# Kernel optimization log

Hardware: AMD Instinct MI355X
Metric: run time of the kernel (lower is better)

Reference implementation:

```python
import jax, jax.numpy as jnp
import numpy as np

E = 65536      # num edges
T = 262144     # num triplets
H = 128        # hidden_channels
D = 64         # int_emb_size
C = 8          # basis_emb_size
NR = 6         # num_radial
NS = 7         # num_spherical
NB = 6         # len(bt_list) = num_BT + 1
BT_LIST = (-1, 0, 1, 2, 3, 4)
NBS = 1        # num_before_skip (also used for after-skip list in original code)


def setup_inputs() -> dict:
    key = jax.random.key(0)
    ks = iter(jax.random.split(key, 40))
    s = 0.05
    p = lambda shape: jax.random.normal(next(ks), shape, dtype=jnp.float32) * s
    inp = dict(
        x=jax.random.normal(next(ks), (E, H), dtype=jnp.float32),
        rbf=jax.random.normal(next(ks), (E, NR), dtype=jnp.float32),
        sbf=jax.random.normal(next(ks), (T, NS * NR), dtype=jnp.float32),
        idx_kj=jax.random.randint(next(ks), (T,), 0, E),
        idx_ji=jax.random.randint(next(ks), (T,), 0, E),
        bt=jax.random.randint(next(ks), (E,), 0, 5),
        lambda_d=1,
        alpha=jnp.float32(0.7),
        # per-branch stacked weights (6 branches)
        W_kj=p((NB, H, H)), b_kj=jnp.zeros((NB, H), jnp.float32),
        W_rbf1=p((NB, NR, C)), W_rbf2=p((NB, C, H)),
        W_sbf1=p((NB, NS * NR, C)), W_sbf2=p((NB, C, D)),
        W_down=p((NB, H, D)),
        W_ji=p((H, H)), b_ji=jnp.zeros((H,), jnp.float32),
        W_up=p((D, H)),
        rb1_w=p((NBS, H, H)), rb1_b=jnp.zeros((NBS, H), jnp.float32),
        rb2_w=p((NBS, H, H)), rb2_b=jnp.zeros((NBS, H), jnp.float32),
        W_lin=p((H, H)), b_lin=jnp.zeros((H,), jnp.float32),
        ra1_w=p((NBS, H, H)), ra1_b=jnp.zeros((NBS, H), jnp.float32),
        ra2_w=p((NBS, H, H)), ra2_b=jnp.zeros((NBS, H), jnp.float32),
    )
    return inp


def reference(x, rbf, sbf, idx_kj, idx_ji, bt, lambda_d, alpha,
              W_kj, b_kj, W_rbf1, W_rbf2, W_sbf1, W_sbf2, W_down,
              W_ji, b_ji, W_up, rb1_w, rb1_b, rb2_w, rb2_b,
              W_lin, b_lin, ra1_w, ra1_b, ra2_w, ra2_b):
    act = jax.nn.silu

    x_ji = act(x @ W_ji + b_ji)                                  # [E,H]

    # per-branch edge transforms, vectorized over the 6 branches (axis b)
    tmp = act(jnp.einsum('eh,bhg->beg', x, W_kj) + b_kj[:, None, :])   # [B,E,H]
    rbf_p = jnp.einsum('er,brc->bec', rbf, W_rbf1)                     # [B,E,C]
    rbf_p = jnp.einsum('bec,bcg->beg', rbf_p, W_rbf2)                  # [B,E,H]
    tmp = tmp * rbf_p
    down = act(jnp.einsum('beh,bhd->bed', tmp, W_down))                # [B,E,D]

    sbf_p = jnp.einsum('ts,bsc->btc', sbf, W_sbf1)                     # [B,T,C]
    sbf_p = jnp.einsum('btc,bcd->btd', sbf_p, W_sbf2)                  # [B,T,D]

    spe = down[:, idx_kj, :] * sbf_p                                   # [B,T,D]

    # last branch scattered with weight alpha
    x_kj_tot = alpha * jax.ops.segment_sum(spe[-1], idx_ji, num_segments=E)

    # per band-type masked scatter with weight (1 - alpha)
    bt_trip = bt[idx_kj]                                               # [T]
    for b, btv in enumerate(BT_LIST):
        m = (bt_trip == btv).astype(x.dtype)[:, None]
        x_kj_tot = x_kj_tot + (1.0 - alpha) * jax.ops.segment_sum(
            spe[b] * m, idx_ji, num_segments=E)

    x_kj = act(x_kj_tot @ W_up)                                        # [E,H]
    h = x_ji + x_kj
    for i in range(rb1_w.shape[0]):
        h = h + act(act(h @ rb1_w[i] + rb1_b[i]) @ rb2_w[i] + rb2_b[i])
    h = act(h @ W_lin + b_lin) + x
    for i in range(ra1_w.shape[0]):
        h = h + act(act(h @ ra1_w[i] + ra1_b[i]) @ ra2_w[i] + ra2_b[i])
    return h
```

## Files before the change

### kernel.cpp

```cpp
#include <hip/hip_runtime.h>
#include <hip/hip_bf16.h>
#include <stdint.h>

typedef __bf16 bf16_t;
typedef bf16_t bf16x8 __attribute__((ext_vector_type(8)));
typedef bf16_t bf16x2 __attribute__((ext_vector_type(2)));
typedef float f32x4 __attribute__((ext_vector_type(4)));

#define E_N 65536
#define T_N 262144
#define CAP 16
#define OVF_MAX T_N

#define ESET_BYTES 61440
#define PSET_BYTES 36864

__device__ __forceinline__ float silu_f(float v) {
  return v / (1.0f + __expf(-v));
}

__device__ __forceinline__ int permrow(int n) {
  return (n & ~31) | ((n & 1) << 4) | ((n & 30) >> 1);
}

__device__ __forceinline__ uint32_t pack_bf16(float a, float b) {
  union { bf16x2 h; uint32_t u; } u;
  u.h[0] = (bf16_t)a; u.h[1] = (bf16_t)b;
  return u.u;
}

__device__ __forceinline__ void g2l16(const void* g, void* l) {
  __builtin_amdgcn_global_load_lds(
      (const __attribute__((address_space(1))) void*)g,
      (__attribute__((address_space(3))) void*)l, 16, 0, 0);
}

template<int CHUNKS>
__device__ __forceinline__ void dma_copy(const char* g, char* l, int wv, int lane) {
#pragma unroll
  for (int c = 0; c < CHUNKS / 4; ++c) {
    const int off = (c * 4 + wv) * 1024 + lane * 16;
    g2l16(g + off, l + off);
  }
}

#define VMCNT0()  asm volatile("s_waitcnt vmcnt(0)" ::: "memory")

template<int KI, int NTJ>
__device__ __forceinline__ void gemm_tile(const bf16_t* A, const bf16_t* B,
                                          int mb, int nb, int l16, int q,
                                          f32x4 (&acc)[2][NTJ]) {
#pragma unroll
  for (int kt = 0; kt < KI; ++kt) {
    const int sw = ((kt * 4 + q) ^ l16) << 3;
    bf16x8 a0 = *(const bf16x8*)(A + ((mb + l16) << 7) + sw);
    bf16x8 a1 = *(const bf16x8*)(A + ((mb + 16 + l16) << 7) + sw);
#pragma unroll
    for (int tj = 0; tj < NTJ; ++tj) {
      bf16x8 b = *(const bf16x8*)(B + ((nb + tj * 16 + l16) << 7) + sw);
      acc[0][tj] = __builtin_amdgcn_mfma_f32_16x16x32_bf16(a0, b, acc[0][tj], 0, 0, 0);
      acc[1][tj] = __builtin_amdgcn_mfma_f32_16x16x32_bf16(a1, b, acc[1][tj], 0, 0, 0);
    }
  }
}

template<int C4>
__device__ __forceinline__ void stage_x(bf16_t* dst, const float* src, int tid) {
  const float4* g = (const float4*)src;
#pragma unroll
  for (int i = tid; i < 64 * C4; i += 256) {
    const int row = i / C4, c4 = i % C4;
    float4 v = g[i];
    bf16_t t[4] = {(bf16_t)v.x, (bf16_t)v.y, (bf16_t)v.z, (bf16_t)v.w};
    *(uint2*)(dst + (row << 7) + ((((c4 >> 1) ^ (row & 15)) << 3) | ((c4 & 1) << 2))) =
        *(const uint2*)t;
  }
}

__global__ void prep_kernel(
    const float* __restrict__ W_ji, const float* __restrict__ W_kj,
    const float* __restrict__ W_down, const float* __restrict__ W_up,
    const float* __restrict__ rb1, const float* __restrict__ rb2,
    const float* __restrict__ W_lin, const float* __restrict__ ra1,
    const float* __restrict__ ra2, const float* __restrict__ W_rbf1,
    const float* __restrict__ W_rbf2,
    const float* __restrict__ b_ji, const float* __restrict__ b_kj,
    const float* __restrict__ rb1_b, const float* __restrict__ rb2_b,
    const float* __restrict__ b_lin, const float* __restrict__ ra1_b,
    const float* __restrict__ ra2_b,
    char* __restrict__ esets, char* __restrict__ psets)
{
  const int tid = threadIdx.x;
  const int blk = blockIdx.x;

  if (blk < 88) {
    const int item = blk * 256 + tid;
    const int m = item >> 11, w = item & 2047;
    const int n = w >> 4, k8 = w & 15;
    const float* src; char* img;
    if (m == 0)      { src = W_ji;             img = esets; }
    else if (m <= 5) { src = W_kj + m * 16384; img = esets + m * ESET_BYTES; }
    else if (m == 6) { src = rb1;   img = psets + 1 * PSET_BYTES; }
    else if (m == 7) { src = rb2;   img = psets + 2 * PSET_BYTES; }
    else if (m == 8) { src = W_lin; img = psets + 3 * PSET_BYTES; }
    else if (m == 9) { src = ra1;   img = psets + 4 * PSET_BYTES; }
    else             { src = ra2;   img = psets + 5 * PSET_BYTES; }
    bf16_t t[8];
#pragma unroll
    for (int j = 0; j < 8; ++j) t[j] = (bf16_t)src[(k8 * 8 + j) * 128 + n];
    const int row = permrow(n);
    *(uint4*)((bf16_t*)img + (row << 7) + ((k8 ^ (row & 15)) << 3)) = *(const uint4*)t;
  } else if (blk < 108) {
    const int item = (blk - 88) * 256 + tid;
    const int m = item >> 10, w = item & 1023;
    const int n = w >> 4, k8 = w & 15;
    const float* src = W_down + (m + 1) * 8192;
    bf16_t* img = (bf16_t*)(esets + (m + 1) * ESET_BYTES + 32768);
    bf16_t t[8];
#pragma unroll
    for (int j = 0; j < 8; ++j) t[j] = (bf16_t)src[(k8 * 8 + j) * 64 + n];
    const int row = permrow(n);
    *(uint4*)(img + (row << 7) + ((k8 ^ (row & 15)) << 3)) = *(const uint4*)t;
  } else if (blk < 112) {
    const int item = (blk - 108) * 256 + tid;
    const int n = item >> 3, k8 = item & 7;
    bf16_t t[8];
#pragma unroll
    for (int j = 0; j < 8; ++j) t[j] = (bf16_t)W_up[(k8 * 8 + j) * 128 + n];
    const int row = permrow(n);
    *(uint4*)((bf16_t*)psets + (row << 7) + ((k8 ^ (row & 15)) << 3)) = *(const uint4*)t;
  } else if (blk < 115) {
    const int o = (blk - 112) * 256 + tid;
    if (o < 640) {
      const int b = o >> 7, n = o & 127;
      bf16_t t[8];
#pragma unroll
      for (int r = 0; r < 6; ++r) {
        const float* w1 = W_rbf1 + (b + 1) * 48 + r * 8;
        const float* w2 = W_rbf2 + (b + 1) * 1024 + n;
        float s = 0.f;
#pragma unroll
        for (int c = 0; c < 8; ++c) s += w1[c] * w2[c * 128];
        t[r] = (bf16_t)s;
      }
      t[6] = (bf16_t)0.f; t[7] = (bf16_t)0.f;
      bf16_t* img = (bf16_t*)(esets + (b + 1) * ESET_BYTES + 49152);
      const int row = permrow(n);
      const uint4 z = {0, 0, 0, 0};
      *(uint4*)(img + row * 40)      = *(const uint4*)t;
      *(uint4*)(img + row * 40 + 8)  = z;
      *(uint4*)(img + row * 40 + 16) = z;
      *(uint4*)(img + row * 40 + 24) = z;
    }
  } else {
    const int n = tid & 127;
    for (int v = (tid >> 7); v < 11; v += 2) {
      float val; char* dst;
      if (v == 0)      { val = b_ji[n];          dst = esets + 59392; }
      else if (v <= 5) { val = b_kj[v * 128 + n]; dst = esets + v * ESET_BYTES + 59392; }
      else {
        const float* bs = (v == 6) ? rb1_b : (v == 7) ? rb2_b :
                          (v == 8) ? b_lin : (v == 9) ? ra1_b : ra2_b;
        val = bs[n]; dst = psets + (v - 5) * PSET_BYTES + 32768;
      }
      ((float*)dst)[n] = val;
    }
  }
}

__global__ __launch_bounds__(256, 1)
void edge_kernel(const float* __restrict__ x, const float* __restrict__ rbf,
                 const char* __restrict__ esets,
                 bf16_t* __restrict__ x_ji_out, bf16_t* __restrict__ down)
{
  __shared__ __align__(16) bf16_t xA[64 * 128];
  __shared__ __align__(16) bf16_t tmpA[64 * 128];
  __shared__ __align__(16) bf16_t rbfA[64 * 40];
  __shared__ __align__(16) char Wset[2][ESET_BYTES];

  const int tid = threadIdx.x;
  const int lane = tid & 63, wv = tid >> 6;
  const int q = lane >> 4, l16 = lane & 15;
  const int mb = (wv >> 1) * 32, nb = (wv & 1) * 64;
  const int R = blockIdx.x * 64;

  stage_x<32>(xA, x + (size_t)R * 128, tid);
  if (tid < 64) {
    const float* rg = rbf + (size_t)(R + tid) * 6;
    bf16_t t[8] = {(bf16_t)rg[0], (bf16_t)rg[1], (bf16_t)rg[2],
                   (bf16_t)rg[3], (bf16_t)rg[4], (bf16_t)rg[5],
                   (bf16_t)0.f, (bf16_t)0.f};
    const uint4 z = {0, 0, 0, 0};
    *(uint4*)(rbfA + tid * 40)      = *(const uint4*)t;
    *(uint4*)(rbfA + tid * 40 + 8)  = z;
    *(uint4*)(rbfA + tid * 40 + 16) = z;
    *(uint4*)(rbfA + tid * 40 + 24) = z;
  }
  VMCNT0();
  dma_copy<60>(esets,              (char*)Wset[0], wv, lane);
  dma_copy<60>(esets + ESET_BYTES, (char*)Wset[1], wv, lane);
  asm volatile("s_waitcnt vmcnt(15)" ::: "memory");
  __syncthreads();

  for (int br = 0; br < 6; ++br) {
    const char* slot = Wset[br & 1];
    const bf16_t* Wm  = (const bf16_t*)slot;
    const bf16_t* Wdn = (const bf16_t*)(slot + 32768);
    const bf16_t* Wcb = (const bf16_t*)(slot + 49152);
    const float* biasS = (const float*)(slot + 59392);

    f32x4 acc[2][4] = {};
    gemm_tile<4, 4>(xA, Wm, mb, nb, l16, q, acc);

    if (br == 0) {
#pragma unroll
      for (int ti = 0; ti < 2; ++ti)
#pragma unroll
        for (int r = 0; r < 4; ++r) {
          const int row = mb + ti * 16 + q * 4 + r;
#pragma unroll
          for (int gl = 0; gl < 2; ++gl) {
            const int col0 = nb + gl * 32 + 2 * l16;
            const float2 b2 = *(const float2*)&biasS[col0];
            *(uint32_t*)&x_ji_out[(size_t)(R + row) * 128 + col0] =
                pack_bf16(silu_f(acc[ti][2 * gl][r] + b2.x),
                          silu_f(acc[ti][2 * gl + 1][r] + b2.y));
          }
        }
    } else {
      f32x4 accr[2][4] = {};
      {
        bf16x8 a0 = *(const bf16x8*)(rbfA + (mb + l16) * 40 + q * 8);
        bf16x8 a1 = *(const bf16x8*)(rbfA + (mb + 16 + l16) * 40 + q * 8);
#pragma unroll
        for (int tj = 0; tj < 4; ++tj) {
          bf16x8 b = *(const bf16x8*)(Wcb + (nb + tj * 16 + l16) * 40 + q * 8);
          accr[0][tj] = __builtin_amdgcn_mfma_f32_16x16x32_bf16(a0, b, accr[0][tj], 0, 0, 0);
          accr[1][tj] = __builtin_amdgcn_mfma_f32_16x16x32_bf16(a1, b, accr[1][tj], 0, 0, 0);
        }
      }
#pragma unroll
      for (int ti = 0; ti < 2; ++ti)
#pragma unroll
        for (int r = 0; r < 4; ++r) {
          const int row = mb + ti * 16 + q * 4 + r;
#pragma unroll
          for (int gl = 0; gl < 2; ++gl) {
            const int col0 = nb + gl * 32 + 2 * l16;
            const float2 b2 = *(const float2*)&biasS[col0];
            const float v0 = silu_f(acc[ti][2 * gl][r] + b2.x) * accr[ti][2 * gl][r];
            const float v1 = silu_f(acc[ti][2 * gl + 1][r] + b2.y) * accr[ti][2 * gl + 1][r];
            *(uint32_t*)&tmpA[(row << 7) + ((((col0 >> 3) ^ (row & 15)) << 3) | (col0 & 7))] =
                pack_bf16(v0, v1);
          }
        }
      __syncthreads();

      const int nb2 = (wv & 1) * 32;
      f32x4 acc2[2][2] = {};
      gemm_tile<4, 2>(tmpA, Wdn, mb, nb2, l16, q, acc2);
#pragma unroll
      for (int ti = 0; ti < 2; ++ti)
#pragma unroll
        for (int r = 0; r < 4; ++r) {
          const int row = mb + ti * 16 + q * 4 + r;
          const int col0 = nb2 + 2 * l16;
          *(uint32_t*)&down[((size_t)(br - 1) * E_N + R + row) * 64 + col0] =
              pack_bf16(silu_f(acc2[ti][0][r]), silu_f(acc2[ti][1][r]));
        }
    }

    VMCNT0();
    __syncthreads();
    if (br < 4)
      dma_copy<60>(esets + (size_t)(br + 2) * ESET_BYTES, (char*)Wset[br & 1], wv, lane);
  }
}

__global__ __launch_bounds__(256, 4)
void c8_kernel(const float* __restrict__ sbf, const int* __restrict__ idx_kj,
               const int* __restrict__ idx_ji, const int* __restrict__ bt,
               const float* __restrict__ Wsbf1,
               float* __restrict__ c8g, uint32_t* __restrict__ meta,
               int* __restrict__ cnt, int* __restrict__ list,
               int* __restrict__ ovf)
{
  __shared__ float s_sbf[64 * 44];
  __shared__ float s_W1[2016];
  __shared__ float s_c8[64 * 16];
  __shared__ int s_bs[64];

  const int tid = threadIdx.x;
  const int base = blockIdx.x * 64;

  for (int i = tid; i < 2016; i += 256) s_W1[i] = Wsbf1[i];
  if (tid < 64) {
    const int t = base + tid;
    const int kj = idx_kj[t];
    const int ji = idx_ji[t];
    const int bs = bt[kj] + 1;
    s_bs[tid] = bs;
    meta[t] = (uint32_t)kj | ((uint32_t)bs << 16);
    const int pos = atomicAdd(&cnt[ji], 1);
    if (pos < CAP) {
      list[ji * CAP + pos] = t;
    } else {
      const int o = atomicAdd(&ovf[0], 1);
      if (o < OVF_MAX) { ovf[2 + 2 * o] = t; ovf[2 + 2 * o + 1] = ji; }
    }
  }
  {
    const float2* sg = (const float2*)(sbf + (size_t)base * 42);
    for (int i = tid; i < 64 * 21; i += 256) {
      const int r = i / 21, c2 = i - r * 21;
      const float2 v = sg[i];
      s_sbf[r * 44 + c2 * 2] = v.x;
      s_sbf[r * 44 + c2 * 2 + 1] = v.y;
    }
  }
  __syncthreads();

  {
    const int i = tid >> 2;
    const int brr = (tid >> 1) & 1;
    const int cg = tid & 1;
    const int b = brr ? s_bs[i] : 5;
    const float* w = &s_W1[b * 336 + cg * 4];
    const float* sb = &s_sbf[i * 44];
    float a0 = 0.f, a1 = 0.f, a2 = 0.f, a3 = 0.f;
#pragma unroll
    for (int s = 0; s < 42; ++s) {
      const float sv = sb[s];
      const float* ws = w + s * 8;
      a0 += sv * ws[0]; a1 += sv * ws[1]; a2 += sv * ws[2]; a3 += sv * ws[3];
    }
    float* dc = &s_c8[i * 16 + brr * 8 + cg * 4];
    dc[0] = a0; dc[1] = a1; dc[2] = a2; dc[3] = a3;
  }
  __syncthreads();

  {
    const float4* s4 = (const float4*)s_c8;
    float4* g4 = (float4*)(c8g + (size_t)base * 16);
    g4[tid] = s4[tid];
  }
}

__global__ __launch_bounds__(256, 8)
void gather_kernel(const int* __restrict__ cnt, const int* __restrict__ list,
                   const uint32_t* __restrict__ meta, const float* __restrict__ c8g,
                   const float* __restrict__ Wsbf2, const bf16_t* __restrict__ down,
                   const float* __restrict__ alpha_p, const int* __restrict__ ovf,
                   float* __restrict__ xkj)
{
  __shared__ float sW2[3072];
  for (int i = threadIdx.x; i < 3072; i += 256) sW2[i] = Wsbf2[i];
  __syncthreads();

  const int e = blockIdx.x * 4 + (threadIdx.x >> 6);
  const int j = threadIdx.x & 63;
  const float alpha = alpha_p[0], oma = 1.f - alpha;
  const float* w5 = &sW2[5 * 512 + j];

  float acc = 0.f;
  int n = cnt[e];
  if (n > CAP) n = CAP;
#pragma unroll 2
  for (int k = 0; k < n; ++k) {
    const int t = __builtin_amdgcn_readfirstlane(list[e * CAP + k]);
    const uint32_t m = __builtin_amdgcn_readfirstlane(meta[t]);
    const int kj = m & 0xffff;
    const int b  = m >> 16;
    const float g5 = (float)down[((size_t)4 * E_N + kj) * 64 + j];
    const float gb = (float)down[((size_t)(b - 1) * E_N + kj) * 64 + j];
    const float* cp = c8g + (size_t)t * 16;
    float d5 = 0.f, db = 0.f;
#pragma unroll
    for (int c = 0; c < 8; ++c) {
      d5 += cp[c]     * w5[c * 64];
      db += cp[8 + c] * sW2[b * 512 + c * 64 + j];
    }
    acc += alpha * g5 * d5 + oma * gb * db;
  }

  const int oc = ovf[0];
  for (int k = 0; k < oc; ++k) {
    const int ji = ovf[2 + 2 * k + 1];
    if (ji != e) continue;
    const int t = ovf[2 + 2 * k];
    const uint32_t m = meta[t];
    const int kj = m & 0xffff;
    const int b  = m >> 16;
    const float g5 = (float)down[((size_t)4 * E_N + kj) * 64 + j];
    const float gb = (float)down[((size_t)(b - 1) * E_N + kj) * 64 + j];
    const float* cp = c8g + (size_t)t * 16;
    float d5 = 0.f, db = 0.f;
#pragma unroll
    for (int c = 0; c < 8; ++c) {
      d5 += cp[c]     * w5[c * 64];
      db += cp[8 + c] * sW2[b * 512 + c * 64 + j];
    }
    acc += alpha * g5 * d5 + oma * gb * db;
  }

  xkj[(size_t)e * 64 + j] = acc;
}

__global__ __launch_bounds__(256, 1)
void epi_kernel(const float* __restrict__ x, const bf16_t* __restrict__ x_ji,
                const float* __restrict__ xkj, const char* __restrict__ psets,
                float* __restrict__ out)
{
  __shared__ __align__(16) bf16_t bufA[64 * 128];
  __shared__ __align__(16) bf16_t bufB[64 * 128];
  __shared__ __align__(16) char Wset[2][PSET_BYTES];

  const int tid = threadIdx.x;
  const int lane = tid & 63, wv = tid >> 6;
  const int q = lane >> 4, l16 = lane & 15;
  const int mb = (wv >> 1) * 32, nb = (wv & 1) * 64;
  const int R = blockIdx.x * 64;

  stage_x<16>(bufA, xkj + (size_t)R * 64, tid);
  VMCNT0();
  dma_copy<36>(psets,              (char*)Wset[0], wv, lane);
  dma_copy<36>(psets + PSET_BYTES, (char*)Wset[1], wv, lane);
  asm volatile("s_waitcnt vmcnt(9)" ::: "memory");
  __syncthreads();

  f32x4 hreg[2][4];
  {
    f32x4 acc[2][4] = {};
    gemm_tile<2, 4>(bufA, (const bf16_t*)Wset[0], mb, nb, l16, q, acc);
#pragma unroll
    for (int ti = 0; ti < 2; ++ti)
#pragma unroll
      for (int r = 0; r < 4; ++r) {
        const int row = mb + ti * 16 + q * 4 + r;
#pragma unroll
        for (int gl = 0; gl < 2; ++gl) {
          const int col0 = nb + gl * 32 + 2 * l16;
          union { uint32_t u; bf16x2 h; } xj;
          xj.u = *(const uint32_t*)&x_ji[(size_t)(R + row) * 128 + col0];
          const float h0 = (float)xj.h[0] + silu_f(acc[ti][2 * gl][r]);
          const float h1 = (float)xj.h[1] + silu_f(acc[ti][2 * gl + 1][r]);
          hreg[ti][2 * gl][r] = h0;
          hreg[ti][2 * gl + 1][r] = h1;
          *(uint32_t*)&bufB[(row << 7) + ((((col0 >> 3) ^ (row & 15)) << 3) | (col0 & 7))] =
              pack_bf16(h0, h1);
        }
      }
  }
  VMCNT0();
  __syncthreads();
  dma_copy<36>(psets + 2 * PSET_BYTES, (char*)Wset[0], wv, lane);

#define EPI_STAGE(K, ASRC, BODY)                                                 \
  {                                                                              \
    const char* slot_ = Wset[(K) & 1];                                           \
    const float* biasS = (const float*)(slot_ + 32768);                          \
    f32x4 acc[2][4] = {};                                                        \
    gemm_tile<4, 4>(ASRC, (const bf16_t*)slot_, mb, nb, l16, q, acc);            \
    _Pragma("unroll")                                                            \
    for (int ti = 0; ti < 2; ++ti)                                               \
      _Pragma("unroll")                                                          \
      for (int r = 0; r < 4; ++r) {                                              \
        const int row = mb + ti * 16 + q * 4 + r;                                \
        _Pragma("unroll")                                                        \
        for (int gl = 0; gl < 2; ++gl) {                                         \
          const int col0 = nb + gl * 32 + 2 * l16;                               \
          const float2 b2 = *(const float2*)&biasS[col0];                        \
          const float g0 = acc[ti][2 * gl][r] + b2.x;                            \
          const float g1 = acc[ti][2 * gl + 1][r] + b2.y;                        \
          BODY                                                                   \
        }                                                                        \
      }                                                                          \
  }                                                                              \
  VMCNT0();                                                                      \
  __syncthreads();                                                               \
  if ((K) + 2 <= 5)                                                              \
    dma_copy<36>(psets + ((K) + 2) * PSET_BYTES, (char*)Wset[(K) & 1], wv, lane);

  EPI_STAGE(1, bufB, {
    *(uint32_t*)&bufA[(row << 7) + ((((col0 >> 3) ^ (row & 15)) << 3) | (col0 & 7))] =
        pack_bf16(silu_f(g0), silu_f(g1));
  })

  EPI_STAGE(2, bufA, {
    const float h0 = hreg[ti][2 * gl][r] + silu_f(g0);
    const float h1 = hreg[ti][2 * gl + 1][r] + silu_f(g1);
    hreg[ti][2 * gl][r] = h0; hreg[ti][2 * gl + 1][r] = h1;
    *(uint32_t*)&bufB[(row << 7) + ((((col0 >> 3) ^ (row & 15)) << 3) | (col0 & 7))] =
        pack_bf16(h0, h1);
  })

  EPI_STAGE(3, bufB, {
    const float2 xv = *(const float2*)&x[(size_t)(R + row) * 128 + col0];
    const float h0 = silu_f(g0) + xv.x;
    const float h1 = silu_f(g1) + xv.y;
    hreg[ti][2 * gl][r] = h0; hreg[ti][2 * gl + 1][r] = h1;
    *(uint32_t*)&bufA[(row << 7) + ((((col0 >> 3) ^ (row & 15)) << 3) | (col0 & 7))] =
        pack_bf16(h0, h1);
  })

  EPI_STAGE(4, bufA, {
    *(uint32_t*)&bufB[(row << 7) + ((((col0 >> 3) ^ (row & 15)) << 3) | (col0 & 7))] =
        pack_bf16(silu_f(g0), silu_f(g1));
  })

  EPI_STAGE(5, bufB, {
    float2 o;
    o.x = hreg[ti][2 * gl][r] + silu_f(g0);
    o.y = hreg[ti][2 * gl + 1][r] + silu_f(g1);
    *(float2*)&out[(size_t)(R + row) * 128 + col0] = o;
  })
#undef EPI_STAGE
}

extern "C" void kernel_launch(void* const* d_in, const int* in_sizes, int n_in,
                              void* d_out, int out_size, void* d_ws, size_t ws_size,
                              hipStream_t stream)
{
  (void)in_sizes; (void)n_in; (void)out_size; (void)ws_size;
  const float* x      = (const float*)d_in[0];
  const float* rbf    = (const float*)d_in[1];
  const float* sbf    = (const float*)d_in[2];
  const int*   idx_kj = (const int*)d_in[3];
  const int*   idx_ji = (const int*)d_in[4];
  const int*   bt     = (const int*)d_in[5];
  const float* alpha  = (const float*)d_in[7];
  const float* W_kj   = (const float*)d_in[8];
  const float* b_kj   = (const float*)d_in[9];
  const float* W_rbf1 = (const float*)d_in[10];
  const float* W_rbf2 = (const float*)d_in[11];
  const float* W_sbf1 = (const float*)d_in[12];
  const float* W_sbf2 = (const float*)d_in[13];
  const float* W_down = (const float*)d_in[14];
  const float* W_ji   = (const float*)d_in[15];
  const float* b_ji   = (const float*)d_in[16];
  const float* W_up   = (const float*)d_in[17];
  const float* rb1_w  = (const float*)d_in[18];
  const float* rb1_b  = (const float*)d_in[19];
  const float* rb2_w  = (const float*)d_in[20];
  const float* rb2_b  = (const float*)d_in[21];
  const float* W_lin  = (const float*)d_in[22];
  const float* b_lin  = (const float*)d_in[23];
  const float* ra1_w  = (const float*)d_in[24];
  const float* ra1_b  = (const float*)d_in[25];
  const float* ra2_w  = (const float*)d_in[26];
  const float* ra2_b  = (const float*)d_in[27];

  char* ws = (char*)d_ws;
  bf16_t* down   = (bf16_t*)(ws);
  bf16_t* x_ji   = (bf16_t*)(ws + 41943040);
  float*  xkj    = (float*) (ws + 58720256);
  char*   esets  = ws + 75497472;
  char*   psets  = ws + 75866112;
  float*    c8g  = (float*)   (ws + 76087296);
  uint32_t* meta = (uint32_t*)(ws + 92864512);
  int*      list = (int*)     (ws + 93913088);
  int*      cnt  = (int*)     (ws + 98107392);
  int*      ovf  = (int*)     (ws + 98369536);

  hipMemsetAsync(cnt, 0, 262144 + 8, stream);
  prep_kernel<<<116, 256, 0, stream>>>(W_ji, W_kj, W_down, W_up, rb1_w, rb2_w,
                                       W_lin, ra1_w, ra2_w, W_rbf1, W_rbf2,
                                       b_ji, b_kj, rb1_b, rb2_b, b_lin,
                                       ra1_b, ra2_b, esets, psets);
  edge_kernel<<<E_N / 64, 256, 0, stream>>>(x, rbf, esets, x_ji, down);
  c8_kernel<<<T_N / 64, 256, 0, stream>>>(sbf, idx_kj, idx_ji, bt, W_sbf1,
                                          c8g, meta, cnt, list, ovf);
  gather_kernel<<<E_N / 4 / 64, 256, 0, stream>>>(cnt, list, meta, c8g, W_sbf2,
                                                  down, alpha, ovf, xkj);
  epi_kernel<<<E_N / 64, 256, 0, stream>>>(x, x_ji, xkj, psets, (float*)d_out);
}
```

Measured before the change: 362.9 us.

## Enlarge edge and epilogue tiles to 128 rows with 512 threads and split weight images

Result: slower. 417.9 us (+15.2%).

```diff
diff --git a/kernel.cpp b/kernel.cpp
--- a/kernel.cpp
+++ b/kernel.cpp
@@ -12,9 +12,6 @@
 #define CAP 16
 #define OVF_MAX T_N
 
-#define ESET_BYTES 61440
-#define PSET_BYTES 36864
-
 __device__ __forceinline__ float silu_f(float v) {
   return v / (1.0f + __expf(-v));
 }
@@ -36,15 +33,22 @@
 }
 
 template<int CHUNKS>
-__device__ __forceinline__ void dma_copy(const char* g, char* l, int wv, int lane) {
-#pragma unroll
-  for (int c = 0; c < CHUNKS / 4; ++c) {
-    const int off = (c * 4 + wv) * 1024 + lane * 16;
+__device__ __forceinline__ void dma8(const char* g, char* l, int wv, int lane) {
+#pragma unroll
+  for (int c = 0; c < CHUNKS / 8; ++c) {
+    const int off = (c * 8 + wv) * 1024 + lane * 16;
     g2l16(g + off, l + off);
   }
 }
 
-#define VMCNT0()  asm volatile("s_waitcnt vmcnt(0)" ::: "memory")
+#define VMCNT0()   asm volatile("s_waitcnt vmcnt(0)" ::: "memory")
+#define S_VMCNT_(n) asm volatile("s_waitcnt vmcnt(" #n ")" ::: "memory")
+#define S_VMCNT(n) S_VMCNT_(n)
+#define BARRIER() do {                                          \
+    asm volatile("s_waitcnt lgkmcnt(0)" ::: "memory");          \
+    __builtin_amdgcn_s_barrier();                               \
+    __builtin_amdgcn_sched_barrier(0);                          \
+  } while (0)
 
 template<int KI, int NTJ>
 __device__ __forceinline__ void gemm_tile(const bf16_t* A, const bf16_t* B,
@@ -64,11 +68,11 @@
   }
 }
 
-template<int C4>
+template<int C4, int NT>
 __device__ __forceinline__ void stage_x(bf16_t* dst, const float* src, int tid) {
   const float4* g = (const float4*)src;
 #pragma unroll
-  for (int i = tid; i < 64 * C4; i += 256) {
+  for (int i = tid; i < 128 * C4; i += NT) {
     const int row = i / C4, c4 = i % C4;
     float4 v = g[i];
     bf16_t t[4] = {(bf16_t)v.x, (bf16_t)v.y, (bf16_t)v.z, (bf16_t)v.w};
@@ -84,11 +88,8 @@
     const float* __restrict__ W_lin, const float* __restrict__ ra1,
     const float* __restrict__ ra2, const float* __restrict__ W_rbf1,
     const float* __restrict__ W_rbf2,
-    const float* __restrict__ b_ji, const float* __restrict__ b_kj,
-    const float* __restrict__ rb1_b, const float* __restrict__ rb2_b,
-    const float* __restrict__ b_lin, const float* __restrict__ ra1_b,
-    const float* __restrict__ ra2_b,
-    char* __restrict__ esets, char* __restrict__ psets)
+    char* __restrict__ wm_img, char* __restrict__ wdn_img,
+    char* __restrict__ pset, bf16_t* __restrict__ wcb)
 {
   const int tid = threadIdx.x;
   const int blk = blockIdx.x;
@@ -98,13 +99,13 @@
     const int m = item >> 11, w = item & 2047;
     const int n = w >> 4, k8 = w & 15;
     const float* src; char* img;
-    if (m == 0)      { src = W_ji;             img = esets; }
-    else if (m <= 5) { src = W_kj + m * 16384; img = esets + m * ESET_BYTES; }
-    else if (m == 6) { src = rb1;   img = psets + 1 * PSET_BYTES; }
-    else if (m == 7) { src = rb2;   img = psets + 2 * PSET_BYTES; }
-    else if (m == 8) { src = W_lin; img = psets + 3 * PSET_BYTES; }
-    else if (m == 9) { src = ra1;   img = psets + 4 * PSET_BYTES; }
-    else             { src = ra2;   img = psets + 5 * PSET_BYTES; }
+    if (m == 0)      { src = W_ji;             img = wm_img; }
+    else if (m <= 5) { src = W_kj + m * 16384; img = wm_img + m * 32768; }
+    else if (m == 6) { src = rb1;   img = pset + 1 * 32768; }
+    else if (m == 7) { src = rb2;   img = pset + 2 * 32768; }
+    else if (m == 8) { src = W_lin; img = pset + 3 * 32768; }
+    else if (m == 9) { src = ra1;   img = pset + 4 * 32768; }
+    else             { src = ra2;   img = pset + 5 * 32768; }
     bf16_t t[8];
 #pragma unroll
     for (int j = 0; j < 8; ++j) t[j] = (bf16_t)src[(k8 * 8 + j) * 128 + n];
@@ -115,7 +116,7 @@
     const int m = item >> 10, w = item & 1023;
     const int n = w >> 4, k8 = w & 15;
     const float* src = W_down + (m + 1) * 8192;
-    bf16_t* img = (bf16_t*)(esets + (m + 1) * ESET_BYTES + 32768);
+    bf16_t* img = (bf16_t*)(wdn_img + m * 16384);
     bf16_t t[8];
 #pragma unroll
     for (int j = 0; j < 8; ++j) t[j] = (bf16_t)src[(k8 * 8 + j) * 64 + n];
@@ -128,8 +129,8 @@
 #pragma unroll
     for (int j = 0; j < 8; ++j) t[j] = (bf16_t)W_up[(k8 * 8 + j) * 128 + n];
     const int row = permrow(n);
-    *(uint4*)((bf16_t*)psets + (row << 7) + ((k8 ^ (row & 15)) << 3)) = *(const uint4*)t;
-  } else if (blk < 115) {
+    *(uint4*)((bf16_t*)pset + (row << 7) + ((k8 ^ (row & 15)) << 3)) = *(const uint4*)t;
+  } else {
     const int o = (blk - 112) * 256 + tid;
     if (o < 640) {
       const int b = o >> 7, n = o & 127;
@@ -144,137 +145,144 @@
         t[r] = (bf16_t)s;
       }
       t[6] = (bf16_t)0.f; t[7] = (bf16_t)0.f;
-      bf16_t* img = (bf16_t*)(esets + (b + 1) * ESET_BYTES + 49152);
-      const int row = permrow(n);
-      const uint4 z = {0, 0, 0, 0};
-      *(uint4*)(img + row * 40)      = *(const uint4*)t;
-      *(uint4*)(img + row * 40 + 8)  = z;
-      *(uint4*)(img + row * 40 + 16) = z;
-      *(uint4*)(img + row * 40 + 24) = z;
-    }
-  } else {
-    const int n = tid & 127;
-    for (int v = (tid >> 7); v < 11; v += 2) {
-      float val; char* dst;
-      if (v == 0)      { val = b_ji[n];          dst = esets + 59392; }
-      else if (v <= 5) { val = b_kj[v * 128 + n]; dst = esets + v * ESET_BYTES + 59392; }
-      else {
-        const float* bs = (v == 6) ? rb1_b : (v == 7) ? rb2_b :
-                          (v == 8) ? b_lin : (v == 9) ? ra1_b : ra2_b;
-        val = bs[n]; dst = psets + (v - 5) * PSET_BYTES + 32768;
-      }
-      ((float*)dst)[n] = val;
-    }
-  }
-}
-
-__global__ __launch_bounds__(256, 1)
+      *(uint4*)(wcb + (b * 128 + n) * 8) = *(const uint4*)t;
+    }
+  }
+}
+
+__global__ __launch_bounds__(512, 2)
 void edge_kernel(const float* __restrict__ x, const float* __restrict__ rbf,
-                 const char* __restrict__ esets,
+                 const char* __restrict__ wm_img, const char* __restrict__ wdn_img,
+                 const bf16_t* __restrict__ wcb,
+                 const float* __restrict__ b_ji, const float* __restrict__ b_kj,
                  bf16_t* __restrict__ x_ji_out, bf16_t* __restrict__ down)
 {
-  __shared__ __align__(16) bf16_t xA[64 * 128];
-  __shared__ __align__(16) bf16_t tmpA[64 * 128];
-  __shared__ __align__(16) bf16_t rbfA[64 * 40];
-  __shared__ __align__(16) char Wset[2][ESET_BYTES];
+  __shared__ __align__(16) bf16_t xA[128 * 128];
+  __shared__ __align__(16) bf16_t tmpA[128 * 128];
+  __shared__ __align__(16) bf16_t Wm[2][128 * 128];
+  __shared__ __align__(16) bf16_t Wdn[64 * 128];
+  __shared__ __align__(16) bf16_t rbfS[128 * 8];
+  __shared__ __align__(16) bf16_t wcbS[5 * 128 * 8];
+  __shared__ __align__(16) float biasLDS[6 * 128];
 
   const int tid = threadIdx.x;
   const int lane = tid & 63, wv = tid >> 6;
   const int q = lane >> 4, l16 = lane & 15;
-  const int mb = (wv >> 1) * 32, nb = (wv & 1) * 64;
-  const int R = blockIdx.x * 64;
-
-  stage_x<32>(xA, x + (size_t)R * 128, tid);
-  if (tid < 64) {
+  const int mb = (wv >> 1) * 32, nb = (wv & 1) * 64, nb2 = (wv & 1) * 32;
+  const int R = blockIdx.x * 128;
+
+  stage_x<32, 512>(xA, x + (size_t)R * 128, tid);
+  if (tid < 128) {
     const float* rg = rbf + (size_t)(R + tid) * 6;
-    bf16_t t[8] = {(bf16_t)rg[0], (bf16_t)rg[1], (bf16_t)rg[2],
-                   (bf16_t)rg[3], (bf16_t)rg[4], (bf16_t)rg[5],
-                   (bf16_t)0.f, (bf16_t)0.f};
-    const uint4 z = {0, 0, 0, 0};
-    *(uint4*)(rbfA + tid * 40)      = *(const uint4*)t;
-    *(uint4*)(rbfA + tid * 40 + 8)  = z;
-    *(uint4*)(rbfA + tid * 40 + 16) = z;
-    *(uint4*)(rbfA + tid * 40 + 24) = z;
-  }
+    const float2 r01 = *(const float2*)(rg);
+    const float2 r23 = *(const float2*)(rg + 2);
+    const float2 r45 = *(const float2*)(rg + 4);
+    bf16_t t[8] = {(bf16_t)r01.x, (bf16_t)r01.y, (bf16_t)r23.x, (bf16_t)r23.y,
+                   (bf16_t)r45.x, (bf16_t)r45.y, (bf16_t)0.f, (bf16_t)0.f};
+    *(uint4*)(rbfS + tid * 8) = *(const uint4*)t;
+  }
+  for (int i = tid; i < 640; i += 512)
+    ((uint4*)wcbS)[i] = ((const uint4*)wcb)[i];
+  for (int i = tid; i < 768; i += 512) {
+    const int b = i >> 7, n = i & 127;
+    biasLDS[i] = (b == 0) ? b_ji[n] : b_kj[b * 128 + n];
+  }
+
   VMCNT0();
-  dma_copy<60>(esets,              (char*)Wset[0], wv, lane);
-  dma_copy<60>(esets + ESET_BYTES, (char*)Wset[1], wv, lane);
-  asm volatile("s_waitcnt vmcnt(15)" ::: "memory");
-  __syncthreads();
-
-  for (int br = 0; br < 6; ++br) {
-    const char* slot = Wset[br & 1];
-    const bf16_t* Wm  = (const bf16_t*)slot;
-    const bf16_t* Wdn = (const bf16_t*)(slot + 32768);
-    const bf16_t* Wcb = (const bf16_t*)(slot + 49152);
-    const float* biasS = (const float*)(slot + 59392);
-
+  dma8<32>(wm_img,          (char*)Wm[0], wv, lane);
+  dma8<32>(wm_img + 32768,  (char*)Wm[1], wv, lane);
+  dma8<16>(wdn_img,         (char*)Wdn,   wv, lane);
+  S_VMCNT(6);
+  BARRIER();
+
+  {
     f32x4 acc[2][4] = {};
-    gemm_tile<4, 4>(xA, Wm, mb, nb, l16, q, acc);
-
-    if (br == 0) {
-#pragma unroll
-      for (int ti = 0; ti < 2; ++ti)
-#pragma unroll
-        for (int r = 0; r < 4; ++r) {
-          const int row = mb + ti * 16 + q * 4 + r;
-#pragma unroll
-          for (int gl = 0; gl < 2; ++gl) {
-            const int col0 = nb + gl * 32 + 2 * l16;
-            const float2 b2 = *(const float2*)&biasS[col0];
-            *(uint32_t*)&x_ji_out[(size_t)(R + row) * 128 + col0] =
-                pack_bf16(silu_f(acc[ti][2 * gl][r] + b2.x),
-                          silu_f(acc[ti][2 * gl + 1][r] + b2.y));
-          }
-        }
-    } else {
-      f32x4 accr[2][4] = {};
-      {
-        bf16x8 a0 = *(const bf16x8*)(rbfA + (mb + l16) * 40 + q * 8);
-        bf16x8 a1 = *(const bf16x8*)(rbfA + (mb + 16 + l16) * 40 + q * 8);
-#pragma unroll
-        for (int tj = 0; tj < 4; ++tj) {
-          bf16x8 b = *(const bf16x8*)(Wcb + (nb + tj * 16 + l16) * 40 + q * 8);
-          accr[0][tj] = __builtin_amdgcn_mfma_f32_16x16x32_bf16(a0, b, accr[0][tj], 0, 0, 0);
-          accr[1][tj] = __builtin_amdgcn_mfma_f32_16x16x32_bf16(a1, b, accr[1][tj], 0, 0, 0);
+    gemm_tile<4, 4>(xA, Wm[0], mb, nb, l16, q, acc);
+    const float* bi = biasLDS;
+#pragma unroll
+    for (int ti = 0; ti < 2; ++ti)
+#pragma unroll
+      for (int r = 0; r < 4; ++r) {
+        const int row = mb + ti * 16 + q * 4 + r;
+#pragma unroll
+        for (int gl = 0; gl < 2; ++gl) {
+          const int col0 = nb + gl * 32 + 2 * l16;
+          const float2 b2 = *(const float2*)&bi[col0];
+          *(uint32_t*)&x_ji_out[(size_t)(R + row) * 128 + col0] =
+              pack_bf16(silu_f(acc[ti][2 * gl][r] + b2.x),
+                        silu_f(acc[ti][2 * gl + 1][r] + b2.y));
         }
       }
-#pragma unroll
-      for (int ti = 0; ti < 2; ++ti)
-#pragma unroll
-        for (int r = 0; r < 4; ++r) {
-          const int row = mb + ti * 16 + q * 4 + r;
-#pragma unroll
-          for (int gl = 0; gl < 2; ++gl) {
-            const int col0 = nb + gl * 32 + 2 * l16;
-            const float2 b2 = *(const float2*)&biasS[col0];
-            const float v0 = silu_f(acc[ti][2 * gl][r] + b2.x) * accr[ti][2 * gl][r];
-            const float v1 = silu_f(acc[ti][2 * gl + 1][r] + b2.y) * accr[ti][2 * gl + 1][r];
-            *(uint32_t*)&tmpA[(row << 7) + ((((col0 >> 3) ^ (row & 15)) << 3) | (col0 & 7))] =
-                pack_bf16(v0, v1);
-          }
-        }
-      __syncthreads();
-
-      const int nb2 = (wv & 1) * 32;
-      f32x4 acc2[2][2] = {};
-      gemm_tile<4, 2>(tmpA, Wdn, mb, nb2, l16, q, acc2);
-#pragma unroll
-      for (int ti = 0; ti < 2; ++ti)
-#pragma unroll
-        for (int r = 0; r < 4; ++r) {
-          const int row = mb + ti * 16 + q * 4 + r;
-          const int col0 = nb2 + 2 * l16;
-          *(uint32_t*)&down[((size_t)(br - 1) * E_N + R + row) * 64 + col0] =
-              pack_bf16(silu_f(acc2[ti][0][r]), silu_f(acc2[ti][1][r]));
-        }
-    }
-
-    VMCNT0();
-    __syncthreads();
-    if (br < 4)
-      dma_copy<60>(esets + (size_t)(br + 2) * ESET_BYTES, (char*)Wset[br & 1], wv, lane);
-  }
+  }
+  S_VMCNT(18);
+  BARRIER();
+  dma8<32>(wm_img + 2 * 32768, (char*)Wm[0], wv, lane);
+
+#define EDGE_BR(BR, VW1, VW2, NWM, NDN)                                          \
+  {                                                                              \
+    f32x4 acc[2][4] = {};                                                        \
+    gemm_tile<4, 4>(xA, Wm[(BR) & 1], mb, nb, l16, q, acc);                      \
+    float wc[2][2][6];                                                           \
+    _Pragma("unroll")                                                            \
+    for (int gl = 0; gl < 2; ++gl)                                               \
+      _Pragma("unroll")                                                          \
+      for (int j = 0; j < 2; ++j) {                                              \
+        const int col = nb + gl * 32 + 2 * l16 + j;                              \
+        bf16x8 w8 = *(const bf16x8*)&wcbS[(((BR) - 1) * 128 + col) * 8];         \
+        _Pragma("unroll")                                                        \
+        for (int c = 0; c < 6; ++c) wc[gl][j][c] = (float)w8[c];                 \
+      }                                                                          \
+    const float* bi = biasLDS + (BR) * 128;                                      \
+    _Pragma("unroll")                                                            \
+    for (int ti = 0; ti < 2; ++ti)                                               \
+      _Pragma("unroll")                                                          \
+      for (int r = 0; r < 4; ++r) {                                              \
+        const int row = mb + ti * 16 + q * 4 + r;                                \
+        bf16x8 rv8 = *(const bf16x8*)&rbfS[row * 8];                             \
+        float rv[6];                                                             \
+        _Pragma("unroll")                                                        \
+        for (int c = 0; c < 6; ++c) rv[c] = (float)rv8[c];                       \
+        _Pragma("unroll")                                                        \
+        for (int gl = 0; gl < 2; ++gl) {                                         \
+          const int col0 = nb + gl * 32 + 2 * l16;                               \
+          const float2 b2 = *(const float2*)&bi[col0];                           \
+          float p0 = 0.f, p1 = 0.f;                                              \
+          _Pragma("unroll")                                                      \
+          for (int c = 0; c < 6; ++c) {                                          \
+            p0 += rv[c] * wc[gl][0][c];                                          \
+            p1 += rv[c] * wc[gl][1][c];                                          \
+          }                                                                      \
+          const float v0 = silu_f(acc[ti][2 * gl][r] + b2.x) * p0;               \
+          const float v1 = silu_f(acc[ti][2 * gl + 1][r] + b2.y) * p1;           \
+          *(uint32_t*)&tmpA[(row << 7) + ((((col0 >> 3) ^ (row & 15)) << 3) | (col0 & 7))] = \
+              pack_bf16(v0, v1);                                                 \
+        }                                                                        \
+      }                                                                          \
+    S_VMCNT(VW1);                                                                \
+    BARRIER();                                                                   \
+    f32x4 acc2[2][2] = {};                                                       \
+    gemm_tile<4, 2>(tmpA, Wdn, mb, nb2, l16, q, acc2);                           \
+    _Pragma("unroll")                                                            \
+    for (int ti = 0; ti < 2; ++ti)                                               \
+      _Pragma("unroll")                                                          \
+      for (int r = 0; r < 4; ++r) {                                              \
+        const int row = mb + ti * 16 + q * 4 + r;                                \
+        const int col0 = nb2 + 2 * l16;                                          \
+        *(uint32_t*)&down[((size_t)((BR) - 1) * E_N + R + row) * 64 + col0] =    \
+            pack_bf16(silu_f(acc2[ti][0][r]), silu_f(acc2[ti][1][r]));           \
+      }                                                                          \
+    S_VMCNT(VW2);                                                                \
+    BARRIER();                                                                   \
+    if ((NDN) >= 0) dma8<16>(wdn_img + (size_t)(NDN) * 16384, (char*)Wdn, wv, lane); \
+    if ((NWM) >= 0) dma8<32>(wm_img + (size_t)(NWM) * 32768, (char*)Wm[(BR) & 1], wv, lane); \
+  }
+
+  EDGE_BR(1, 20, 8, 3, 1)
+  EDGE_BR(2,  4, 8, 4, 2)
+  EDGE_BR(3,  4, 8, 5, 3)
+  EDGE_BR(4,  4, 8, -1, 4)
+  EDGE_BR(5,  0, 63, -1, -1)
+#undef EDGE_BR
 }
 
 __global__ __launch_bounds__(256, 4)
@@ -406,32 +414,42 @@
   xkj[(size_t)e * 64 + j] = acc;
 }
 
-__global__ __launch_bounds__(256, 1)
+__global__ __launch_bounds__(512, 2)
 void epi_kernel(const float* __restrict__ x, const bf16_t* __restrict__ x_ji,
-                const float* __restrict__ xkj, const char* __restrict__ psets,
+                const float* __restrict__ xkj, const char* __restrict__ pset,
+                const float* __restrict__ rb1_b, const float* __restrict__ rb2_b,
+                const float* __restrict__ lin_b, const float* __restrict__ ra1_b,
+                const float* __restrict__ ra2_b,
                 float* __restrict__ out)
 {
-  __shared__ __align__(16) bf16_t bufA[64 * 128];
-  __shared__ __align__(16) bf16_t bufB[64 * 128];
-  __shared__ __align__(16) char Wset[2][PSET_BYTES];
+  __shared__ __align__(16) bf16_t bufA[128 * 128];
+  __shared__ __align__(16) bf16_t bufB[128 * 128];
+  __shared__ __align__(16) bf16_t Wset[2][128 * 128];
+  __shared__ __align__(16) float biasLDS[5 * 128];
 
   const int tid = threadIdx.x;
   const int lane = tid & 63, wv = tid >> 6;
   const int q = lane >> 4, l16 = lane & 15;
   const int mb = (wv >> 1) * 32, nb = (wv & 1) * 64;
-  const int R = blockIdx.x * 64;
-
-  stage_x<16>(bufA, xkj + (size_t)R * 64, tid);
+  const int R = blockIdx.x * 128;
+
+  stage_x<16, 512>(bufA, xkj + (size_t)R * 64, tid);
+  for (int i = tid; i < 640; i += 512) {
+    const int b = i >> 7, n = i & 127;
+    const float* bs = (b == 0) ? rb1_b : (b == 1) ? rb2_b :
+                      (b == 2) ? lin_b : (b == 3) ? ra1_b : ra2_b;
+    biasLDS[i] = bs[n];
+  }
   VMCNT0();
-  dma_copy<36>(psets,              (char*)Wset[0], wv, lane);
-  dma_copy<36>(psets + PSET_BYTES, (char*)Wset[1], wv, lane);
-  asm volatile("s_waitcnt vmcnt(9)" ::: "memory");
-  __syncthreads();
+  dma8<32>(pset,          (char*)Wset[0], wv, lane);
+  dma8<32>(pset + 32768,  (char*)Wset[1], wv, lane);
+  S_VMCNT(4);
+  BARRIER();
 
   f32x4 hreg[2][4];
   {
     f32x4 acc[2][4] = {};
-    gemm_tile<2, 4>(bufA, (const bf16_t*)Wset[0], mb, nb, l16, q, acc);
+    gemm_tile<2, 4>(bufA, Wset[0], mb, nb, l16, q, acc);
 #pragma unroll
     for (int ti = 0; ti < 2; ++ti)
 #pragma unroll
@@ -452,15 +470,14 @@
       }
   }
   VMCNT0();
-  __syncthreads();
-  dma_copy<36>(psets + 2 * PSET_BYTES, (char*)Wset[0], wv, lane);
+  BARRIER();
+  dma8<32>(pset + 2 * 32768, (char*)Wset[0], wv, lane);
 
 #define EPI_STAGE(K, ASRC, BODY)                                                 \
   {                                                                              \
-    const char* slot_ = Wset[(K) & 1];                                           \
-    const float* biasS = (const float*)(slot_ + 32768);                          \
+    const float* biasS = biasLDS + ((K) - 1) * 128;                              \
     f32x4 acc[2][4] = {};                                                        \
-    gemm_tile<4, 4>(ASRC, (const bf16_t*)slot_, mb, nb, l16, q, acc);            \
+    gemm_tile<4, 4>(ASRC, Wset[(K) & 1], mb, nb, l16, q, acc);                   \
     _Pragma("unroll")                                                            \
     for (int ti = 0; ti < 2; ++ti)                                               \
       _Pragma("unroll")                                                          \
@@ -477,9 +494,9 @@
       }                                                                          \
   }                                                                              \
   VMCNT0();                                                                      \
-  __syncthreads();                                                               \
+  BARRIER();                                                                     \
   if ((K) + 2 <= 5)                                                              \
-    dma_copy<36>(psets + ((K) + 2) * PSET_BYTES, (char*)Wset[(K) & 1], wv, lane);
+    dma8<32>(pset + (size_t)((K) + 2) * 32768, (char*)Wset[(K) & 1], wv, lane);
 
   EPI_STAGE(1, bufB, {
     *(uint32_t*)&bufA[(row << 7) + ((((col0 >> 3) ^ (row & 15)) << 3) | (col0 & 7))] =
@@ -554,23 +571,27 @@
   bf16_t* down   = (bf16_t*)(ws);
   bf16_t* x_ji   = (bf16_t*)(ws + 41943040);
   float*  xkj    = (float*) (ws + 58720256);
-  char*   esets  = ws + 75497472;
-  char*   psets  = ws + 75866112;
-  float*    c8g  = (float*)   (ws + 76087296);
-  uint32_t* meta = (uint32_t*)(ws + 92864512);
-  int*      list = (int*)     (ws + 93913088);
-  int*      cnt  = (int*)     (ws + 98107392);
-  int*      ovf  = (int*)     (ws + 98369536);
+  char*   wm_img = ws + 75497472;
+  char*   wdn_img= ws + 75694080;
+  char*   pset   = ws + 75776000;
+  bf16_t* wcb    = (bf16_t*)(ws + 75972608);
+  float*    c8g  = (float*)   (ws + 75982848);
+  uint32_t* meta = (uint32_t*)(ws + 92760064);
+  int*      list = (int*)     (ws + 93808640);
+  int*      cnt  = (int*)     (ws + 98002944);
+  int*      ovf  = (int*)     (ws + 98265088);
 
   hipMemsetAsync(cnt, 0, 262144 + 8, stream);
-  prep_kernel<<<116, 256, 0, stream>>>(W_ji, W_kj, W_down, W_up, rb1_w, rb2_w,
+  prep_kernel<<<115, 256, 0, stream>>>(W_ji, W_kj, W_down, W_up, rb1_w, rb2_w,
                                        W_lin, ra1_w, ra2_w, W_rbf1, W_rbf2,
-                                       b_ji, b_kj, rb1_b, rb2_b, b_lin,
-                                       ra1_b, ra2_b, esets, psets);
-  edge_kernel<<<E_N / 64, 256, 0, stream>>>(x, rbf, esets, x_ji, down);
+                                       wm_img, wdn_img, pset, wcb);
+  edge_kernel<<<E_N / 128, 512, 0, stream>>>(x, rbf, wm_img, wdn_img, wcb,
+                                             b_ji, b_kj, x_ji, down);
   c8_kernel<<<T_N / 64, 256, 0, stream>>>(sbf, idx_kj, idx_ji, bt, W_sbf1,
                                           c8g, meta, cnt, list, ovf);
   gather_kernel<<<E_N / 4 / 64, 256, 0, stream>>>(cnt, list, meta, c8g, W_sbf2,
                                                   down, alpha, ovf, xkj);
-  epi_kernel<<<E_N / 64, 256, 0, stream>>>(x, x_ji, xkj, psets, (float*)d_out);
-}
+  epi_kernel<<<E_N / 128, 512, 0, stream>>>(x, x_ji, xkj, pset,
+                                            rb1_b, rb2_b, b_lin, ra1_b, ra2_b,
+                                            (float*)d_out);
+}
```
